# Kernel tuning notes

Hardware: AMD Instinct MI355X
Metric: run time of the kernel (lower is better)

Reference implementation:

```python
import jax, jax.numpy as jnp
import numpy as np
import math

B, S, D = 4, 2048, 1024
H = 16
HD = D // H  # 64
NEG_INF = -1e9


def setup_inputs() -> dict:
    key = jax.random.key(0)
    k1, k2, k3, k4, k5 = jax.random.split(key, 5)
    x = jax.random.normal(k1, (B, S, D), dtype=jnp.float32)
    # rotary frequencies (theta = 10000), shape (S, HD//2)
    inv_freq = 1.0 / (10000.0 ** (jnp.arange(0, HD, 2, dtype=jnp.float32) / HD))
    t = jnp.arange(S, dtype=jnp.float32)
    freqs = jnp.outer(t, inv_freq)  # (S, HD//2)
    freqs_cos = jnp.cos(freqs)
    freqs_sin = jnp.sin(freqs)
    # causal additive mask (1,1,S,S)
    causal = jnp.tril(jnp.ones((S, S), dtype=bool))
    mask = jnp.where(causal, 0.0, NEG_INF).astype(jnp.float32)[None, None]
    scale = 0.02
    wq = jax.random.normal(k2, (D, D), dtype=jnp.float32) * scale
    wk = jax.random.normal(k3, (D, D), dtype=jnp.float32) * scale
    wv = jax.random.normal(k4, (D, D), dtype=jnp.float32) * scale
    wo = jax.random.normal(k5, (D, D), dtype=jnp.float32) * scale
    return {"x": x, "freqs_cos": freqs_cos, "freqs_sin": freqs_sin,
            "mask": mask, "wq": wq, "wk": wk, "wv": wv, "wo": wo}


def _apply_rotary(t, cos, sin):
    # t: (B,S,H,HD); cos/sin: (S, HD//2) broadcast as (1,S,1,HD//2)
    tr = t.reshape(*t.shape[:-1], HD // 2, 2)
    t0, t1 = tr[..., 0], tr[..., 1]
    c = cos[None, :, None, :]
    s = sin[None, :, None, :]
    o0 = t0 * c - t1 * s
    o1 = t0 * s + t1 * c
    return jnp.stack([o0, o1], axis=-1).reshape(t.shape)


def reference(x, freqs_cos, freqs_sin, mask, wq, wk, wv, wo):
    bsz, seqlen, _ = x.shape
    xq = (x @ wq).reshape(bsz, seqlen, H, HD)
    xk = (x @ wk).reshape(bsz, seqlen, H, HD)
    xv = (x @ wv).reshape(bsz, seqlen, H, HD)
    xq = _apply_rotary(xq, freqs_cos, freqs_sin)
    xk = _apply_rotary(xk, freqs_cos, freqs_sin)
    # (B,H,S,HD)
    xq = xq.transpose(0, 2, 1, 3)
    xk = xk.transpose(0, 2, 1, 3)
    xv = xv.transpose(0, 2, 1, 3)
    scores = jnp.einsum('bhqd,bhkd->bhqk', xq, xk) / math.sqrt(HD)
    scores = scores + mask
    probs = jax.nn.softmax(scores.astype(jnp.float32), axis=-1).astype(xq.dtype)
    # dropout is identity in eval mode
    out = jnp.einsum('bhqk,bhkd->bhqd', probs, xv)
    out = out.transpose(0, 2, 1, 3).reshape(bsz, seqlen, H * HD)
    return out @ wo
```

## Files before the change

### kernel.cpp

```cpp
#include <hip/hip_runtime.h>
#include <stdint.h>

typedef short short8 __attribute__((ext_vector_type(8)));
typedef float f32x4 __attribute__((ext_vector_type(4)));
typedef float f32x16 __attribute__((ext_vector_type(16)));
typedef unsigned int u32x4 __attribute__((ext_vector_type(4)));
typedef float float4e __attribute__((ext_vector_type(4)));
typedef unsigned short u16;

#define BB 4
#define SS 2048
#define DD 1024
#define HH 16
#define MM (BB*SS)

__device__ __forceinline__ u16 f2bf(float f) {
    unsigned u = __float_as_uint(f);
    u += 0x7FFFu + ((u >> 16) & 1u);
    return (u16)(u >> 16);
}
__device__ __forceinline__ float bf2f(u16 h) {
    return __uint_as_float(((unsigned)h) << 16);
}
__device__ __forceinline__ unsigned cvtpk(float a, float b) {
    unsigned r;
    asm("v_cvt_pk_bf16_f32 %0, %1, %2" : "=v"(r) : "v"(a), "v"(b));
    return r;
}
__device__ __forceinline__ void gload16(const void* g, void* l) {
    __builtin_amdgcn_global_load_lds(
        (const __attribute__((address_space(1))) unsigned int*)(uintptr_t)g,
        (__attribute__((address_space(3))) unsigned int*)(unsigned)(uintptr_t)l,
        16, 0, 0);
}
__device__ __forceinline__ bool tens_is_bf(const u16* mref) { return mref[1] == 0xCE6Eu; }
#define PIPE_BAR() do { __builtin_amdgcn_sched_barrier(0); __builtin_amdgcn_s_barrier(); __builtin_amdgcn_sched_barrier(0); } while(0)

__global__ __launch_bounds__(256) void cvt_x(const void* xin, u16* xb, const u16* mref) {
    bool isbf = tens_is_bf(mref);
    size_t i = (size_t)blockIdx.x * 256 + threadIdx.x;
    if (isbf) {
        ((u32x4*)xb)[i] = ((const u32x4*)xin)[i];
    } else {
        const float4e* src = (const float4e*)xin;
        float4e a = src[2*i], b = src[2*i+1];
        u32x4 o;
        o[0] = (unsigned)f2bf(a[0]) | ((unsigned)f2bf(a[1]) << 16);
        o[1] = (unsigned)f2bf(a[2]) | ((unsigned)f2bf(a[3]) << 16);
        o[2] = (unsigned)f2bf(b[0]) | ((unsigned)f2bf(b[1]) << 16);
        o[3] = (unsigned)f2bf(b[2]) | ((unsigned)f2bf(b[3]) << 16);
        ((u32x4*)xb)[i] = o;
    }
}

__global__ __launch_bounds__(256) void trw(const void* w0, const void* w1, const void* w2, const void* w3,
                                           u16* wt, const u16* mref) {
    bool isbf = tens_is_bf(mref);
    const void* w = (blockIdx.z == 0) ? w0 : (blockIdx.z == 1) ? w1 : (blockIdx.z == 2) ? w2 : w3;
    u16* out = wt + (size_t)blockIdx.z * (DD*DD);
    __shared__ float t[32][33];
    int tx = threadIdx.x & 31, ty = threadIdx.x >> 5;
    int n0 = blockIdx.x * 32, k0 = blockIdx.y * 32;
#pragma unroll
    for (int i = 0; i < 4; ++i) {
        int k = k0 + ty*4 + i;
        float v = isbf ? bf2f(((const u16*)w)[(size_t)k*DD + n0 + tx])
                       : ((const float*)w)[(size_t)k*DD + n0 + tx];
        t[ty*4 + i][tx] = v;
    }
    __syncthreads();
#pragma unroll
    for (int i = 0; i < 4; ++i)
        out[(size_t)(n0 + ty*4 + i)*DD + k0 + tx] = f2bf(t[tx][ty*4 + i]);
}

#define QSCALE 0.1803368801111204f
template<int MODE>
__global__ __launch_bounds__(256) void gemm128(const u16* __restrict__ A, const u16* __restrict__ Bt,
                                               void* Cout, const void* fcos, const void* fsin,
                                               const u16* mref, float oscale) {
    constexpr int SMEMB = (MODE == 2) ? 36864 : 32768;
    __shared__ __align__(16) unsigned char smem[SMEMB];
    int tid = threadIdx.x;
    int w = tid >> 6, l = tid & 63, lo = l & 15, hi = l >> 4;
    int wm = w >> 1, wn = w & 1;
    int m0 = blockIdx.x * 128, n0 = blockIdx.y * 128;

    f32x4 acc[4][4] = {};

    auto stage = [&](int buf, int t) {
        int k0 = t * 32;
#pragma unroll
        for (int i = 0; i < 2; ++i) {
            int o = (i*256 + tid) * 16;
            int row = o >> 6, inb = o & 63;
            int sw  = inb ^ ((row & 3) << 4);
            gload16((const char*)A + ((size_t)(m0 + row)*DD + k0)*2 + sw,
                    smem + buf*16384 + (i*256 + (tid & ~63))*16);
            gload16((const char*)Bt + ((size_t)(n0 + row)*DD + k0)*2 + sw,
                    smem + buf*16384 + 8192 + (i*256 + (tid & ~63))*16);
        }
    };

    stage(0, 0);
    __syncthreads();
    int cur = 0;
    const int NT = DD / 32;
    for (int t = 0; t < NT; ++t) {
        if (t + 1 < NT) stage(cur ^ 1, t + 1);
        const char* Ab = (const char*)(smem + cur*16384);
        const char* Bb = Ab + 8192;
        short8 af[4], bfr[4];
#pragma unroll
        for (int mi = 0; mi < 4; ++mi) {
            int r = wm*64 + mi*16 + lo;
            int ib = hi * 16;
            af[mi] = *(const short8*)(Ab + r*64 + (ib ^ ((r & 3) << 4)));
        }
#pragma unroll
        for (int ni = 0; ni < 4; ++ni) {
            int r = wn*64 + ni*16 + lo;
            int ib = hi * 16;
            bfr[ni] = *(const short8*)(Bb + r*64 + (ib ^ ((r & 3) << 4)));
        }
        __builtin_amdgcn_s_setprio(1);
#pragma unroll
        for (int mi = 0; mi < 4; ++mi)
#pragma unroll
            for (int ni = 0; ni < 4; ++ni)
                acc[mi][ni] = __builtin_amdgcn_mfma_f32_16x16x32_bf16(af[mi], bfr[ni], acc[mi][ni], 0, 0, 0);
        __builtin_amdgcn_s_setprio(0);
        __syncthreads();
        cur ^= 1;
    }

    if (MODE == 0) {
        bool fbf = (((const u16*)fcos)[0] == 0x3F80u);
        u16* outp = (u16*)Cout;
#pragma unroll
        for (int mi = 0; mi < 4; ++mi)
#pragma unroll
            for (int ni = 0; ni < 4; ++ni)
#pragma unroll
                for (int r = 0; r < 4; ++r) {
                    int gm = m0 + wm*64 + mi*16 + hi*4 + r;
                    int gc = n0 + wn*64 + ni*16 + lo;
                    float v  = acc[mi][ni][r];
                    float vp = __shfl_xor(v, 1);
                    int s = gm & (SS-1), d = gc & 63, i2 = d >> 1;
                    float co, sn;
                    if (fbf) { co = bf2f(((const u16*)fcos)[s*32 + i2]); sn = bf2f(((const u16*)fsin)[s*32 + i2]); }
                    else     { co = ((const float*)fcos)[s*32 + i2];     sn = ((const float*)fsin)[s*32 + i2]; }
                    float o = (gc & 1) ? (vp*sn + v*co) : (v*co - vp*sn);
                    o *= oscale;
                    int b = gm >> 11, h = gc >> 6;
                    outp[((((size_t)b*HH + h)*SS + s) << 6) + d] = f2bf(o);
                }
    } else if (MODE == 2) {
        __syncthreads();
        u16* vs = (u16*)smem + w * (64*72);
#pragma unroll
        for (int ni = 0; ni < 4; ++ni) {
            int d = ni*16 + lo;
#pragma unroll
            for (int mi = 0; mi < 4; ++mi)
#pragma unroll
                for (int rr = 0; rr < 2; ++rr) {
                    unsigned pk = (unsigned)f2bf(acc[mi][ni][2*rr]) | ((unsigned)f2bf(acc[mi][ni][2*rr+1]) << 16);
                    *(unsigned*)(vs + d*72 + mi*16 + hi*4 + rr*2) = pk;
                }
        }
        asm volatile("s_waitcnt lgkmcnt(0)" ::: "memory");
        int bq = (m0 + wm*64) >> 11;
        int s_base = (m0 + wm*64) & (SS-1);
        int h = (n0 + wn*64) >> 6;
        u16* outp = (u16*)Cout;
#pragma unroll
        for (int p = 0; p < 8; ++p) {
            int idx = p*64 + l;
            int row = idx >> 3, ch = idx & 7;
            short8 vv = *(const short8*)(vs + row*72 + ch*8);
            *(short8*)(outp + (((size_t)bq*HH + h)*64 + row)*SS + s_base + ch*8) = vv;
        }
    } else {
        bool isbf = tens_is_bf(mref);
#pragma unroll
        for (int mi = 0; mi < 4; ++mi)
#pragma unroll
            for (int ni = 0; ni < 4; ++ni)
#pragma unroll
                for (int r = 0; r < 4; ++r) {
                    int gm = m0 + wm*64 + mi*16 + hi*4 + r;
                    int gc = n0 + wn*64 + ni*16 + lo;
                    float v = acc[mi][ni][r];
                    if (isbf) ((u16*)Cout)[(size_t)gm*DD + gc] = f2bf(v);
                    else      ((float*)Cout)[(size_t)gm*DD + gc] = v;
                }
    }
}

__global__ __launch_bounds__(256) void attn(const u16* __restrict__ Q, const u16* __restrict__ K,
                                            const u16* __restrict__ VT, u16* __restrict__ AO) {
    __shared__ __align__(16) u16 Kl[3][64*64];
    __shared__ __align__(16) u16 Vl[3][64*64];
    int bh = blockIdx.x;
    int qt = (gridDim.y - 1) - blockIdx.y;
    int tid = threadIdx.x, w = tid >> 6, l = tid & 63;
    int l31 = l & 31, hi5 = l >> 5;
    const u16* Qb = Q  + (size_t)bh * SS * 64;
    const u16* Kb = K  + (size_t)bh * SS * 64;
    const u16* Vb = VT + (size_t)bh * 64 * SS;
    int q0w = qt*128 + w*32;
    int q   = q0w + l31;

    short8 qf[4];
#pragma unroll
    for (int kc = 0; kc < 4; ++kc)
        qf[kc] = *(const short8*)(Qb + (size_t)q*64 + kc*16 + hi5*8);

    int loff[2][4];
#pragma unroll
    for (int g = 0; g < 2; ++g)
#pragma unroll
        for (int kc = 0; kc < 4; ++kc) {
            int row = g*32 + l31;
            int ib = kc*32 + hi5*16;
            loff[g][kc] = row*128 + (ib ^ ((row & 7) << 4));
        }

    f32x16 oacc[2] = {};
    float m_ = -1e30f, l_ = 0.f;

    auto stage = [&](int buf, int kt) {
        const char* Kt = (const char*)(Kb + (size_t)kt*64*64);
        const char* Vt = (const char*)Vb + (size_t)kt*128;
#pragma unroll
        for (int i = 0; i < 2; ++i) {
            int idx = i*256 + tid;
            int row = idx >> 3, inb = (idx & 7) * 16;
            int sw = inb ^ ((row & 7) << 4);
            gload16(Kt + row*128 + sw,            (char*)Kl[buf] + (i*256 + (tid & ~63))*16);
            gload16(Vt + (size_t)row*(SS*2) + sw, (char*)Vl[buf] + (i*256 + (tid & ~63))*16);
        }
    };

    int nkt = 2*qt + 2;
    stage(0, 0);
    stage(1, 1);
    asm volatile("s_waitcnt vmcnt(4)" ::: "memory");
    PIPE_BAR();

    int cur = 0;
    for (int kt = 0; kt < nkt; ++kt) {
        int nx = cur + 2; if (nx >= 3) nx -= 3;
        bool pre = (kt + 2 < nkt);
        if (pre) stage(nx, kt + 2);

        if (kt*64 <= q0w + 31) {
            const char* Kc = (const char*)Kl[cur];
            const char* Vc = (const char*)Vl[cur];
            f32x16 sc[2] = {};
            __builtin_amdgcn_s_setprio(1);
#pragma unroll
            for (int kvt = 0; kvt < 2; ++kvt) {
                short8 kf[4];
#pragma unroll
                for (int kc = 0; kc < 4; ++kc)
                    kf[kc] = *(const short8*)(Kc + loff[kvt][kc]);
#pragma unroll
                for (int kc = 0; kc < 4; ++kc)
                    sc[kvt] = __builtin_amdgcn_mfma_f32_32x32x16_bf16(kf[kc], qf[kc], sc[kvt], 0, 0, 0);
            }
            __builtin_amdgcn_s_setprio(0);

            if (kt*64 + 63 > q0w) {
#pragma unroll
                for (int kvt = 0; kvt < 2; ++kvt)
#pragma unroll
                    for (int rg = 0; rg < 16; ++rg) {
                        int kv = kt*64 + kvt*32 + (rg & 3) + 8*(rg >> 2) + 4*hi5;
                        if (kv > q) sc[kvt][rg] = -1e9f;
                    }
            }

            float m8[8];
#pragma unroll
            for (int j = 0; j < 8; ++j)
                m8[j] = fmaxf(fmaxf(sc[0][j], sc[0][j+8]), fmaxf(sc[1][j], sc[1][j+8]));
            float mx = fmaxf(fmaxf(fmaxf(m8[0], m8[1]), fmaxf(m8[2], m8[3])),
                             fmaxf(fmaxf(m8[4], m8[5]), fmaxf(m8[6], m8[7])));
            mx = fmaxf(mx, __shfl_xor(mx, 32));
            if (!__all(mx <= m_ + 8.f)) {
                float mn = fmaxf(m_, mx);
                float al = exp2f(m_ - mn);
                m_ = mn;
                l_ *= al;
#pragma unroll
                for (int dt = 0; dt < 2; ++dt)
#pragma unroll
                    for (int rg = 0; rg < 16; ++rg) oacc[dt][rg] *= al;
            }
#pragma unroll
            for (int kvt = 0; kvt < 2; ++kvt)
#pragma unroll
                for (int rg = 0; rg < 16; ++rg)
                    sc[kvt][rg] = exp2f(sc[kvt][rg] - m_);
            float s8[8];
#pragma unroll
            for (int j = 0; j < 8; ++j)
                s8[j] = (sc[0][j] + sc[0][j+8]) + (sc[1][j] + sc[1][j+8]);
            float rs = ((s8[0] + s8[1]) + (s8[2] + s8[3])) + ((s8[4] + s8[5]) + (s8[6] + s8[7]));
            rs += __shfl_xor(rs, 32);
            l_ += rs;

            short8 pa[4];
#pragma unroll
            for (int kc = 0; kc < 4; ++kc) {
                const int kvt = kc >> 1;
                const int base = (kc & 1) * 8;
                unsigned A0 = cvtpk(sc[kvt][base + 0], sc[kvt][base + 1]);
                unsigned A1 = cvtpk(sc[kvt][base + 2], sc[kvt][base + 3]);
                unsigned B0 = cvtpk(sc[kvt][base + 4], sc[kvt][base + 5]);
                unsigned B1 = cvtpk(sc[kvt][base + 6], sc[kvt][base + 7]);
                asm("v_permlane32_swap_b32 %0, %1" : "+v"(A0), "+v"(B0));
                asm("v_permlane32_swap_b32 %0, %1" : "+v"(A1), "+v"(B1));
                u32x4 pk; pk[0] = A0; pk[1] = A1; pk[2] = B0; pk[3] = B1;
                pa[kc] = __builtin_bit_cast(short8, pk);
            }

            __builtin_amdgcn_s_setprio(1);
#pragma unroll
            for (int dt = 0; dt < 2; ++dt) {
                short8 vf[4];
#pragma unroll
                for (int kc = 0; kc < 4; ++kc)
                    vf[kc] = *(const short8*)(Vc + loff[dt][kc]);
#pragma unroll
                for (int kc = 0; kc < 4; ++kc)
                    oacc[dt] = __builtin_amdgcn_mfma_f32_32x32x16_bf16(vf[kc], pa[kc], oacc[dt], 0, 0, 0);
            }
            __builtin_amdgcn_s_setprio(0);
        }

        if (pre) asm volatile("s_waitcnt vmcnt(4)" ::: "memory");
        else     asm volatile("s_waitcnt vmcnt(0)" ::: "memory");
        PIPE_BAR();
        cur = (cur == 2) ? 0 : cur + 1;
    }

    int b = bh >> 4, h = bh & 15;
    float inv = 1.0f / l_;
    u16* aor = AO + (size_t)(b*SS + q)*DD + h*64;
#pragma unroll
    for (int dt = 0; dt < 2; ++dt)
#pragma unroll
        for (int j = 0; j < 8; ++j) {
            int r0 = 2*j, r1 = 2*j + 1;
            int d = dt*32 + (r0 & 3) + 8*(r0 >> 2) + 4*hi5;
            unsigned pk = (unsigned)f2bf(oacc[dt][r0] * inv) | ((unsigned)f2bf(oacc[dt][r1] * inv) << 16);
            *(unsigned*)(aor + d) = pk;
        }
}

extern "C" void kernel_launch(void* const* d_in, const int* in_sizes, int n_in,
                              void* d_out, int out_size, void* d_ws, size_t ws_size,
                              hipStream_t stream) {
    const void* x    = d_in[0];
    const void* fcos = d_in[1];
    const void* fsin = d_in[2];
    const u16*  mref = (const u16*)d_in[3];
    const void* wq   = d_in[4];
    const void* wk   = d_in[5];
    const void* wv   = d_in[6];
    const void* wo   = d_in[7];

    u16* ws = (u16*)d_ws;
    const size_t XB = (size_t)MM * DD;
    const size_t WT = (size_t)DD * DD;
    u16* xb  = ws;
    u16* wt  = ws + XB;
    u16* qb  = ws + XB + 4*WT;
    u16* kb  = qb + XB;
    u16* vtb = kb + XB;

    cvt_x<<<4096, 256, 0, stream>>>(x, xb, mref);
    trw<<<dim3(32, 32, 4), 256, 0, stream>>>(wq, wk, wv, wo, wt, mref);
    gemm128<0><<<dim3(64, 8), 256, 0, stream>>>(xb, wt,        qb,  fcos, fsin, mref, QSCALE);
    gemm128<0><<<dim3(64, 8), 256, 0, stream>>>(xb, wt + WT,   kb,  fcos, fsin, mref, 1.0f);
    gemm128<2><<<dim3(64, 8), 256, 0, stream>>>(xb, wt + 2*WT, vtb, fcos, fsin, mref, 1.0f);
    attn<<<dim3(64, 16), 256, 0, stream>>>(qb, kb, vtb, xb);
    gemm128<3><<<dim3(64, 8), 256, 0, stream>>>(xb, wt + 3*WT, d_out, fcos, fsin, mref, 1.0f);
}
```

Before: 206.5 us.

## Widen GEMM K-tile to 64 and revert attention to double-buffered staging

The GEMM now stages 64-wide K slices (64 KB LDS, 8-way XOR swizzle) and issues two MFMA k-steps per barrier, which halves the number of loop iterations and barriers. In exchange, LDS per block rises to 64 KB, which may cut occupancy. Attention drops from a triple buffer with fine-grained vmcnt waits to a double buffer with plain __syncthreads. That lowers its LDS use but exposes more load latency, since only one tile is prefetched ahead.

```diff
diff --git a/kernel.cpp b/kernel.cpp
--- a/kernel.cpp
+++ b/kernel.cpp
@@ -34,7 +34,6 @@
         16, 0, 0);
 }
 __device__ __forceinline__ bool tens_is_bf(const u16* mref) { return mref[1] == 0xCE6Eu; }
-#define PIPE_BAR() do { __builtin_amdgcn_sched_barrier(0); __builtin_amdgcn_s_barrier(); __builtin_amdgcn_sched_barrier(0); } while(0)
 
 __global__ __launch_bounds__(256) void cvt_x(const void* xin, u16* xb, const u16* mref) {
     bool isbf = tens_is_bf(mref);
@@ -79,8 +78,7 @@
 __global__ __launch_bounds__(256) void gemm128(const u16* __restrict__ A, const u16* __restrict__ Bt,
                                                void* Cout, const void* fcos, const void* fsin,
                                                const u16* mref, float oscale) {
-    constexpr int SMEMB = (MODE == 2) ? 36864 : 32768;
-    __shared__ __align__(16) unsigned char smem[SMEMB];
+    __shared__ __align__(16) unsigned char smem[65536];
     int tid = threadIdx.x;
     int w = tid >> 6, l = tid & 63, lo = l & 15, hi = l >> 4;
     int wm = w >> 1, wn = w & 1;
@@ -89,46 +87,51 @@
     f32x4 acc[4][4] = {};
 
     auto stage = [&](int buf, int t) {
-        int k0 = t * 32;
-#pragma unroll
-        for (int i = 0; i < 2; ++i) {
-            int o = (i*256 + tid) * 16;
-            int row = o >> 6, inb = o & 63;
-            int sw  = inb ^ ((row & 3) << 4);
+        int k0 = t * 64;
+#pragma unroll
+        for (int i = 0; i < 4; ++i) {
+            int idx = i*256 + tid;
+            int row = idx >> 3;
+            int inb = (idx & 7) * 16;
+            int sw  = inb ^ ((row & 7) << 4);
             gload16((const char*)A + ((size_t)(m0 + row)*DD + k0)*2 + sw,
-                    smem + buf*16384 + (i*256 + (tid & ~63))*16);
+                    smem + buf*32768 + (i*256 + (tid & ~63))*16);
             gload16((const char*)Bt + ((size_t)(n0 + row)*DD + k0)*2 + sw,
-                    smem + buf*16384 + 8192 + (i*256 + (tid & ~63))*16);
+                    smem + buf*32768 + 16384 + (i*256 + (tid & ~63))*16);
         }
     };
 
     stage(0, 0);
     __syncthreads();
     int cur = 0;
-    const int NT = DD / 32;
+    const int NT = DD / 64;
     for (int t = 0; t < NT; ++t) {
         if (t + 1 < NT) stage(cur ^ 1, t + 1);
-        const char* Ab = (const char*)(smem + cur*16384);
-        const char* Bb = Ab + 8192;
-        short8 af[4], bfr[4];
+        const char* Ab = (const char*)(smem + cur*32768);
+        const char* Bb = Ab + 16384;
+        short8 af[4][2], bfr[4][2];
 #pragma unroll
         for (int mi = 0; mi < 4; ++mi) {
             int r = wm*64 + mi*16 + lo;
-            int ib = hi * 16;
-            af[mi] = *(const short8*)(Ab + r*64 + (ib ^ ((r & 3) << 4)));
+#pragma unroll
+            for (int ks = 0; ks < 2; ++ks)
+                af[mi][ks] = *(const short8*)(Ab + r*128 + ((ks*64 + hi*16) ^ ((r & 7) << 4)));
         }
 #pragma unroll
         for (int ni = 0; ni < 4; ++ni) {
             int r = wn*64 + ni*16 + lo;
-            int ib = hi * 16;
-            bfr[ni] = *(const short8*)(Bb + r*64 + (ib ^ ((r & 3) << 4)));
+#pragma unroll
+            for (int ks = 0; ks < 2; ++ks)
+                bfr[ni][ks] = *(const short8*)(Bb + r*128 + ((ks*64 + hi*16) ^ ((r & 7) << 4)));
         }
         __builtin_amdgcn_s_setprio(1);
 #pragma unroll
-        for (int mi = 0; mi < 4; ++mi)
-#pragma unroll
-            for (int ni = 0; ni < 4; ++ni)
-                acc[mi][ni] = __builtin_amdgcn_mfma_f32_16x16x32_bf16(af[mi], bfr[ni], acc[mi][ni], 0, 0, 0);
+        for (int ks = 0; ks < 2; ++ks)
+#pragma unroll
+            for (int mi = 0; mi < 4; ++mi)
+#pragma unroll
+                for (int ni = 0; ni < 4; ++ni)
+                    acc[mi][ni] = __builtin_amdgcn_mfma_f32_16x16x32_bf16(af[mi][ks], bfr[ni][ks], acc[mi][ni], 0, 0, 0);
         __builtin_amdgcn_s_setprio(0);
         __syncthreads();
         cur ^= 1;
@@ -201,8 +204,8 @@
 
 __global__ __launch_bounds__(256) void attn(const u16* __restrict__ Q, const u16* __restrict__ K,
                                             const u16* __restrict__ VT, u16* __restrict__ AO) {
-    __shared__ __align__(16) u16 Kl[3][64*64];
-    __shared__ __align__(16) u16 Vl[3][64*64];
+    __shared__ __align__(16) u16 Kl[2][64*64];
+    __shared__ __align__(16) u16 Vl[2][64*64];
     int bh = blockIdx.x;
     int qt = (gridDim.y - 1) - blockIdx.y;
     int tid = threadIdx.x, w = tid >> 6, l = tid & 63;
@@ -246,15 +249,11 @@
 
     int nkt = 2*qt + 2;
     stage(0, 0);
-    stage(1, 1);
-    asm volatile("s_waitcnt vmcnt(4)" ::: "memory");
-    PIPE_BAR();
-
+    __syncthreads();
     int cur = 0;
+
     for (int kt = 0; kt < nkt; ++kt) {
-        int nx = cur + 2; if (nx >= 3) nx -= 3;
-        bool pre = (kt + 2 < nkt);
-        if (pre) stage(nx, kt + 2);
+        if (kt + 1 < nkt) stage(cur ^ 1, kt + 1);
 
         if (kt*64 <= q0w + 31) {
             const char* Kc = (const char*)Kl[cur];
@@ -342,10 +341,8 @@
             __builtin_amdgcn_s_setprio(0);
         }
 
-        if (pre) asm volatile("s_waitcnt vmcnt(4)" ::: "memory");
-        else     asm volatile("s_waitcnt vmcnt(0)" ::: "memory");
-        PIPE_BAR();
-        cur = (cur == 2) ? 0 : cur + 1;
+        __syncthreads();
+        cur ^= 1;
     }
 
     int b = bh >> 4, h = bh & 15;
```

After: 204.7 us. About the same (-0.9%).
